# Performance work log

Measured on AMD Instinct MI355X. Metric: run time of the kernel, lower is better.

## Reference

```python
import jax, jax.numpy as jnp
import numpy as np


def setup_inputs() -> dict:
    key = jax.random.key(0)
    ks = jax.random.split(key, 4)
    B, H, W, C = 4, 64, 64, 256
    d = C // 8
    x = jax.random.normal(ks[0], (B, H, W, C), dtype=jnp.float32)
    wq = jax.random.normal(ks[1], (C, d), dtype=jnp.float32) * (1.0 / np.sqrt(C))
    wk = jax.random.normal(ks[2], (C, d), dtype=jnp.float32) * (1.0 / np.sqrt(C))
    wv = jax.random.normal(ks[3], (C, C), dtype=jnp.float32) * (1.0 / np.sqrt(C))
    bq = jnp.zeros((d,), dtype=jnp.float32)
    bk = jnp.zeros((d,), dtype=jnp.float32)
    bv = jnp.zeros((C,), dtype=jnp.float32)
    return {"x": x, "wq": wq, "bq": bq, "wk": wk, "bk": bk, "wv": wv, "bv": bv}


def reference(x, wq, bq, wk, bk, wv, bv):
    # x: [B, H, W, C] (channels-last, as in Keras Conv2D default)
    B, H, W, C = x.shape
    N = H * W
    xf = x.reshape(B, N, C)                      # 1x1 conv == per-pixel matmul
    q = xf @ wq + bq                             # [B, N, C//8]
    k = xf @ wk + bk                             # [B, N, C//8]
    v = xf @ wv + bv                             # [B, N, C]
    # NOTE: original module applies NO 1/sqrt(d) scaling.
    attn = jax.nn.softmax(jnp.einsum('bnd,bmd->bnm', q, k), axis=-1)  # [B, N, N]
    out = jnp.einsum('bnm,bmc->bnc', attn, v)    # [B, N, C]
    return out.reshape(B, H, W, C) + x
```

## Files before the change

### kernel.cpp

```cpp
#include <hip/hip_runtime.h>
#include <stdint.h>

typedef _Float16 f16;
typedef f16 half8 __attribute__((ext_vector_type(8)));
typedef f16 half4 __attribute__((ext_vector_type(4)));
typedef float floatx4 __attribute__((ext_vector_type(4)));

#define MFMA_F16(A, B, Cc) __builtin_amdgcn_mfma_f32_16x16x32_f16((A), (B), (Cc), 0, 0, 0)

static constexpr int NB  = 4;
static constexpr int NN  = 4096;
static constexpr int NC  = 256;
static constexpr int ND  = 32;
static constexpr int PIX = NB * NN;
static constexpr int NS  = 4;
static constexpr int KS  = NN / NS;

__device__ f16 g_WbT[320 * 256];
__device__ f16 g_Qh[(size_t)PIX * ND];
__device__ f16 g_Kh[(size_t)PIX * ND];
__device__ f16 g_VbT[(size_t)NB * NC * NN];
__device__ f16 g_Of[(size_t)NS * PIX * NC];
__device__ float g_m[NS * PIX];
__device__ float g_l[NS * PIX];

__device__ inline void gl2lds16(const f16* g, f16* l) {
  __builtin_amdgcn_global_load_lds(
      (const __attribute__((address_space(1))) void*)g,
      (__attribute__((address_space(3))) void*)l, 16, 0, 0);
}

__global__ __launch_bounds__(256) void prep_weights(const float* __restrict__ wq,
                                                    const float* __restrict__ wk,
                                                    const float* __restrict__ wv) {
  const int tid = blockIdx.x * 256 + threadIdx.x;
  if (tid >= 320 * 256) return;
  const int j = tid >> 8;
  const int k = tid & 255;
  float v;
  if (j < 32)      v = wq[k * 32 + j];
  else if (j < 64) v = wk[k * 32 + (j - 32)];
  else             v = wv[k * 256 + (j - 64)];
  g_WbT[j * 256 + k] = (f16)v;
}

__global__ __launch_bounds__(256) void proj_qkv(const float* __restrict__ x,
                                                const float* __restrict__ bq,
                                                const float* __restrict__ bk,
                                                const float* __restrict__ bv) {
  __shared__ f16 xs[64 * 32];
  __shared__ f16 wsT[320 * 32];
  __shared__ f16 vt[256 * 64];

  const int tid  = threadIdx.x;
  const int lane = tid & 63;
  const int wid  = tid >> 6;
  const int qd   = lane >> 4;
  const int c16  = lane & 15;
  const int p0   = blockIdx.x * 64;
  const floatx4 zero4 = {0.f, 0.f, 0.f, 0.f};

  floatx4 acc[20];
#pragma unroll
  for (int i = 0; i < 20; ++i) acc[i] = zero4;

  for (int kk = 0; kk < 256; kk += 32) {
    {
      const int r = tid >> 2, g = tid & 3;
      const floatx4* s4 = (const floatx4*)(x + (size_t)(p0 + r) * NC + kk + g * 8);
      const floatx4 xa = s4[0], xb = s4[1];
      half8 h;
      h[0] = (f16)xa[0]; h[1] = (f16)xa[1]; h[2] = (f16)xa[2]; h[3] = (f16)xa[3];
      h[4] = (f16)xb[0]; h[5] = (f16)xb[1]; h[6] = (f16)xb[2]; h[7] = (f16)xb[3];
      *(half8*)&xs[r * 32 + g * 8] = h;
    }
#pragma unroll
    for (int i = 0; i < 10; ++i) {
      const int cid = tid + 256 * i;
      const int j = cid >> 3, m = cid & 7;
      *(half4*)&wsT[j * 32 + m * 4] = *(const half4*)&g_WbT[j * 256 + kk + m * 4];
    }
    __syncthreads();
    const half8 a = *(const half8*)&xs[(wid * 16 + c16) * 32 + qd * 8];
#pragma unroll
    for (int nt = 0; nt < 20; ++nt) {
      const half8 bfr = *(const half8*)&wsT[(nt * 16 + c16) * 32 + qd * 8];
      acc[nt] = MFMA_F16(a, bfr, acc[nt]);
    }
    __syncthreads();
  }

#pragma unroll
  for (int nt = 0; nt < 20; ++nt) {
    const int j = nt * 16 + c16;
    const float bias = (j < 32) ? bq[j] : (j < 64) ? bk[j - 32] : bv[j - 64];
#pragma unroll
    for (int r = 0; r < 4; ++r) {
      const int rl = wid * 16 + qd * 4 + r;
      const int p  = p0 + rl;
      const float val = acc[nt][r] + bias;
      if (j < 32) {
        g_Qh[(size_t)p * ND + j] = (f16)(val * 1.44269504f);
      } else if (j < 64) {
        g_Kh[(size_t)p * ND + (j - 32)] = (f16)val;
      } else {
        vt[(j - 64) * 64 + rl] = (f16)val;
      }
    }
  }
  __syncthreads();
  const int b  = p0 >> 12;
  const int n0 = p0 & (NN - 1);
#pragma unroll
  for (int i = 0; i < 16; ++i) {
    const int cid = tid + 256 * i;
    const int c = cid >> 4, m = cid & 15;
    *(half4*)(g_VbT + ((size_t)(b * NC + c)) * NN + n0 + m * 4) =
        *(const half4*)&vt[c * 64 + m * 4];
  }
}

__global__ __launch_bounds__(256, 2) void attn_split(void) {
  __shared__ f16 vsT[256 * 64];
  __shared__ f16 ps[4][2][16 * 64];

  const int tid  = threadIdx.x;
  const int lane = tid & 63;
  const int wid  = tid >> 6;
  const int qd   = lane >> 4;
  const int c16  = lane & 15;
  const int b    = blockIdx.y;
  const int s    = blockIdx.z;
  const int q0   = blockIdx.x * 128 + wid * 32;
  const int sx7  = c16 & 7;
  const floatx4 zero4 = {0.f, 0.f, 0.f, 0.f};

  const int vrow = wid * 64 + (lane >> 3);
  const int vchk = (lane & 7) ^ ((lane >> 3) & 7);
  const f16* vlane = g_VbT + ((size_t)(b * NC + vrow)) * NN + vchk * 8;
  f16* vdst = &vsT[(size_t)wid * 4096 + (size_t)0];

  half8 qf[2];
#pragma unroll
  for (int g = 0; g < 2; ++g)
    qf[g] = *(const half8*)(g_Qh + ((size_t)(b * NN + q0 + g * 16 + c16)) * ND + qd * 8);

  floatx4 acc[2][16];
#pragma unroll
  for (int g = 0; g < 2; ++g)
#pragma unroll
    for (int i = 0; i < 16; ++i) acc[g][i] = zero4;
  float m_i[2] = {-1e30f, -1e30f};
  float l_p[2] = {0.f, 0.f};

  const int kbeg = s * KS, kend = (s + 1) * KS;

#pragma unroll
  for (int i = 0; i < 8; ++i)
    gl2lds16(vlane + kbeg + i * 8 * NN, vdst + i * 512);
  half8 kreg[4];
#pragma unroll
  for (int a = 0; a < 4; ++a)
    kreg[a] = *(const half8*)(g_Kh + ((size_t)(b * NN + kbeg + a * 16 + c16)) * ND + qd * 8);

  for (int k0 = kbeg; k0 < kend; k0 += 64) {
    floatx4 st[2][4];
#pragma unroll
    for (int g = 0; g < 2; ++g)
#pragma unroll
      for (int a = 0; a < 4; ++a) st[g][a] = MFMA_F16(kreg[a], qf[g], zero4);

    float tm[2];
#pragma unroll
    for (int g = 0; g < 2; ++g) {
      float t0 = fmaxf(fmaxf(st[g][0][0], st[g][0][1]), fmaxf(st[g][0][2], st[g][0][3]));
      float t1 = fmaxf(fmaxf(st[g][1][0], st[g][1][1]), fmaxf(st[g][1][2], st[g][1][3]));
      float t2 = fmaxf(fmaxf(st[g][2][0], st[g][2][1]), fmaxf(st[g][2][2], st[g][2][3]));
      float t3 = fmaxf(fmaxf(st[g][3][0], st[g][3][1]), fmaxf(st[g][3][2], st[g][3][3]));
      tm[g] = fmaxf(fmaxf(t0, t1), fmaxf(t2, t3));
    }
    if (__any(tm[0] > m_i[0] || tm[1] > m_i[1])) {
#pragma unroll
      for (int g = 0; g < 2; ++g) {
        float tr = tm[g];
        tr = fmaxf(tr, __shfl_xor(tr, 16));
        tr = fmaxf(tr, __shfl_xor(tr, 32));
        const float m_new = (tr > m_i[g]) ? tr + 5.0f : m_i[g];
        const float alpha = exp2f(m_i[g] - m_new);
        m_i[g] = m_new;
        l_p[g] *= alpha;
        float a4[4];
#pragma unroll
        for (int r = 0; r < 4; ++r) a4[r] = __shfl(alpha, qd * 4 + r);
#pragma unroll
        for (int ct = 0; ct < 16; ++ct)
#pragma unroll
          for (int r = 0; r < 4; ++r) acc[g][ct][r] *= a4[r];
      }
    }

#pragma unroll
    for (int g = 0; g < 2; ++g) {
      float ts = 0.f;
#pragma unroll
      for (int a = 0; a < 4; ++a) {
        half4 h;
#pragma unroll
        for (int r = 0; r < 4; ++r) {
          const float p = exp2f(st[g][a][r] - m_i[g]);
          ts += p;
          h[r] = (f16)p;
        }
        const int pc = ((a * 2 + (qd >> 1)) ^ sx7) * 8 + (qd & 1) * 4;
        *(half4*)&ps[wid][g][c16 * 64 + pc] = h;
      }
      l_p[g] += ts;
    }

    __syncthreads();

    const int k0n = (k0 + 64 < kend) ? (k0 + 64) : kbeg;
    half8 knew[4];
#pragma unroll
    for (int a = 0; a < 4; ++a)
      knew[a] = *(const half8*)(g_Kh + ((size_t)(b * NN + k0n + a * 16 + c16)) * ND + qd * 8);

    half8 pa[2][2];
#pragma unroll
    for (int g = 0; g < 2; ++g)
#pragma unroll
      for (int kh = 0; kh < 2; ++kh)
        pa[g][kh] = *(const half8*)&ps[wid][g][c16 * 64 + ((kh * 4 + qd) ^ sx7) * 8];
#pragma unroll
    for (int ct = 0; ct < 16; ++ct) {
#pragma unroll
      for (int kh = 0; kh < 2; ++kh) {
        const half8 bfr =
            *(const half8*)&vsT[(ct * 16 + c16) * 64 + ((kh * 4 + qd) ^ sx7) * 8];
        acc[0][ct] = MFMA_F16(pa[0][kh], bfr, acc[0][ct]);
        acc[1][ct] = MFMA_F16(pa[1][kh], bfr, acc[1][ct]);
      }
    }
    __syncthreads();

    if (k0 + 64 < kend) {
#pragma unroll
      for (int i = 0; i < 8; ++i)
        gl2lds16(vlane + (k0 + 64) + i * 8 * NN, vdst + i * 512);
    }
#pragma unroll
    for (int a = 0; a < 4; ++a) kreg[a] = knew[a];
  }

#pragma unroll
  for (int g = 0; g < 2; ++g) {
    float l = l_p[g];
    l += __shfl_xor(l, 16);
    l += __shfl_xor(l, 32);
    if (qd == 0) {
      const int row = b * NN + q0 + g * 16 + c16;
      g_m[s * PIX + row] = m_i[g];
      g_l[s * PIX + row] = l;
    }
    float linv[4];
#pragma unroll
    for (int r = 0; r < 4; ++r) linv[r] = 1.0f / __shfl(l, qd * 4 + r);
#pragma unroll
    for (int ct = 0; ct < 16; ++ct)
#pragma unroll
      for (int r = 0; r < 4; ++r) {
        const int qrow = q0 + g * 16 + qd * 4 + r;
        const int c = ct * 16 + c16;
        g_Of[((size_t)(s * PIX + b * NN + qrow)) * NC + c] = (f16)(acc[g][ct][r] * linv[r]);
      }
  }
}

__global__ __launch_bounds__(256) void combine(const float* __restrict__ x,
                                               float* __restrict__ out) {
  const int tid  = threadIdx.x;
  const int lane = tid & 63;
  const int wid  = tid >> 6;
  const int row  = blockIdx.x * 4 + wid;
  const int c    = lane * 4;

  float m[NS], l[NS], M = -1e30f;
#pragma unroll
  for (int s = 0; s < NS; ++s) {
    m[s] = g_m[s * PIX + row];
    l[s] = g_l[s * PIX + row];
    M = fmaxf(M, m[s]);
  }
  float w[NS], den = 0.f;
#pragma unroll
  for (int s = 0; s < NS; ++s) { w[s] = l[s] * exp2f(m[s] - M); den += w[s]; }
  const float inv = 1.0f / den;

  float a0 = 0.f, a1 = 0.f, a2 = 0.f, a3 = 0.f;
#pragma unroll
  for (int s = 0; s < NS; ++s) {
    const half4 h = *(const half4*)&g_Of[((size_t)(s * PIX + row)) * NC + c];
    const float ws = w[s] * inv;
    a0 += ws * (float)h[0];
    a1 += ws * (float)h[1];
    a2 += ws * (float)h[2];
    a3 += ws * (float)h[3];
  }
  const floatx4 xv = *(const floatx4*)&x[(size_t)row * NC + c];
  floatx4 o;
  o[0] = a0 + xv[0]; o[1] = a1 + xv[1]; o[2] = a2 + xv[2]; o[3] = a3 + xv[3];
  *(floatx4*)&out[(size_t)row * NC + c] = o;
}

extern "C" void kernel_launch(void* const* d_in, const int* in_sizes, int n_in,
                              void* d_out, int out_size, void* d_ws, size_t ws_size,
                              hipStream_t stream) {
  (void)in_sizes; (void)n_in; (void)d_ws; (void)ws_size; (void)out_size;
  const float* x  = (const float*)d_in[0];
  const float* wq = (const float*)d_in[1];
  const float* bq = (const float*)d_in[2];
  const float* wk = (const float*)d_in[3];
  const float* bk = (const float*)d_in[4];
  const float* wv = (const float*)d_in[5];
  const float* bv = (const float*)d_in[6];
  float* out = (float*)d_out;

  hipLaunchKernelGGL(prep_weights, dim3(320), dim3(256), 0, stream, wq, wk, wv);
  hipLaunchKernelGGL(proj_qkv, dim3(256), dim3(256), 0, stream, x, bq, bk, bv);
  hipLaunchKernelGGL(attn_split, dim3(NN / 128, NB, NS), dim3(256), 0, stream);
  hipLaunchKernelGGL(combine, dim3(PIX / 4), dim3(256), 0, stream, x, out);
}
```

Measured before the change: 166.2 us.

## Halve per-wave query rows in attention to raise occupancy

```diff
diff --git a/kernel.cpp b/kernel.cpp
--- a/kernel.cpp
+++ b/kernel.cpp
@@ -120,9 +120,9 @@
   }
 }
 
-__global__ __launch_bounds__(256, 2) void attn_split(void) {
+__global__ __launch_bounds__(256, 4) void attn_split(void) {
   __shared__ f16 vsT[256 * 64];
-  __shared__ f16 ps[4][2][16 * 64];
+  __shared__ f16 ps[4][16 * 64];
 
   const int tid  = threadIdx.x;
   const int lane = tid & 63;
@@ -131,27 +131,23 @@
   const int c16  = lane & 15;
   const int b    = blockIdx.y;
   const int s    = blockIdx.z;
-  const int q0   = blockIdx.x * 128 + wid * 32;
+  const int q0   = blockIdx.x * 64 + wid * 16;
   const int sx7  = c16 & 7;
   const floatx4 zero4 = {0.f, 0.f, 0.f, 0.f};
 
   const int vrow = wid * 64 + (lane >> 3);
   const int vchk = (lane & 7) ^ ((lane >> 3) & 7);
   const f16* vlane = g_VbT + ((size_t)(b * NC + vrow)) * NN + vchk * 8;
-  f16* vdst = &vsT[(size_t)wid * 4096 + (size_t)0];
-
-  half8 qf[2];
-#pragma unroll
-  for (int g = 0; g < 2; ++g)
-    qf[g] = *(const half8*)(g_Qh + ((size_t)(b * NN + q0 + g * 16 + c16)) * ND + qd * 8);
-
-  floatx4 acc[2][16];
-#pragma unroll
-  for (int g = 0; g < 2; ++g)
-#pragma unroll
-    for (int i = 0; i < 16; ++i) acc[g][i] = zero4;
-  float m_i[2] = {-1e30f, -1e30f};
-  float l_p[2] = {0.f, 0.f};
+  f16* vdst = &vsT[(size_t)wid * 4096];
+
+  const half8 qf =
+      *(const half8*)(g_Qh + ((size_t)(b * NN + q0 + c16)) * ND + qd * 8);
+
+  floatx4 acc[16];
+#pragma unroll
+  for (int i = 0; i < 16; ++i) acc[i] = zero4;
+  float m_i = -1e30f;
+  float l_p = 0.f;
 
   const int kbeg = s * KS, kend = (s + 1) * KS;
 
@@ -164,81 +160,65 @@
     kreg[a] = *(const half8*)(g_Kh + ((size_t)(b * NN + kbeg + a * 16 + c16)) * ND + qd * 8);
 
   for (int k0 = kbeg; k0 < kend; k0 += 64) {
-    floatx4 st[2][4];
-#pragma unroll
-    for (int g = 0; g < 2; ++g)
-#pragma unroll
-      for (int a = 0; a < 4; ++a) st[g][a] = MFMA_F16(kreg[a], qf[g], zero4);
-
-    float tm[2];
-#pragma unroll
-    for (int g = 0; g < 2; ++g) {
-      float t0 = fmaxf(fmaxf(st[g][0][0], st[g][0][1]), fmaxf(st[g][0][2], st[g][0][3]));
-      float t1 = fmaxf(fmaxf(st[g][1][0], st[g][1][1]), fmaxf(st[g][1][2], st[g][1][3]));
-      float t2 = fmaxf(fmaxf(st[g][2][0], st[g][2][1]), fmaxf(st[g][2][2], st[g][2][3]));
-      float t3 = fmaxf(fmaxf(st[g][3][0], st[g][3][1]), fmaxf(st[g][3][2], st[g][3][3]));
-      tm[g] = fmaxf(fmaxf(t0, t1), fmaxf(t2, t3));
-    }
-    if (__any(tm[0] > m_i[0] || tm[1] > m_i[1])) {
-#pragma unroll
-      for (int g = 0; g < 2; ++g) {
-        float tr = tm[g];
-        tr = fmaxf(tr, __shfl_xor(tr, 16));
-        tr = fmaxf(tr, __shfl_xor(tr, 32));
-        const float m_new = (tr > m_i[g]) ? tr + 5.0f : m_i[g];
-        const float alpha = exp2f(m_i[g] - m_new);
-        m_i[g] = m_new;
-        l_p[g] *= alpha;
-        float a4[4];
-#pragma unroll
-        for (int r = 0; r < 4; ++r) a4[r] = __shfl(alpha, qd * 4 + r);
-#pragma unroll
-        for (int ct = 0; ct < 16; ++ct)
-#pragma unroll
-          for (int r = 0; r < 4; ++r) acc[g][ct][r] *= a4[r];
+    floatx4 st[4];
+#pragma unroll
+    for (int a = 0; a < 4; ++a) st[a] = MFMA_F16(kreg[a], qf, zero4);
+
+    float t0 = fmaxf(fmaxf(st[0][0], st[0][1]), fmaxf(st[0][2], st[0][3]));
+    float t1 = fmaxf(fmaxf(st[1][0], st[1][1]), fmaxf(st[1][2], st[1][3]));
+    float t2 = fmaxf(fmaxf(st[2][0], st[2][1]), fmaxf(st[2][2], st[2][3]));
+    float t3 = fmaxf(fmaxf(st[3][0], st[3][1]), fmaxf(st[3][2], st[3][3]));
+    const float tm = fmaxf(fmaxf(t0, t1), fmaxf(t2, t3));
+    if (__any(tm > m_i)) {
+      float tr = tm;
+      tr = fmaxf(tr, __shfl_xor(tr, 16));
+      tr = fmaxf(tr, __shfl_xor(tr, 32));
+      const float m_new = (tr > m_i) ? tr + 5.0f : m_i;
+      const float alpha = exp2f(m_i - m_new);
+      m_i = m_new;
+      l_p *= alpha;
+      float a4[4];
+#pragma unroll
+      for (int r = 0; r < 4; ++r) a4[r] = __shfl(alpha, qd * 4 + r);
+#pragma unroll
+      for (int ct = 0; ct < 16; ++ct)
+#pragma unroll
+        for (int r = 0; r < 4; ++r) acc[ct][r] *= a4[r];
+    }
+
+    float ts = 0.f;
+#pragma unroll
+    for (int a = 0; a < 4; ++a) {
+      half4 h;
+#pragma unroll
+      for (int r = 0; r < 4; ++r) {
+        const float p = exp2f(st[a][r] - m_i);
+        ts += p;
+        h[r] = (f16)p;
       }
-    }
-
-#pragma unroll
-    for (int g = 0; g < 2; ++g) {
-      float ts = 0.f;
-#pragma unroll
-      for (int a = 0; a < 4; ++a) {
-        half4 h;
-#pragma unroll
-        for (int r = 0; r < 4; ++r) {
-          const float p = exp2f(st[g][a][r] - m_i[g]);
-          ts += p;
-          h[r] = (f16)p;
-        }
-        const int pc = ((a * 2 + (qd >> 1)) ^ sx7) * 8 + (qd & 1) * 4;
-        *(half4*)&ps[wid][g][c16 * 64 + pc] = h;
-      }
-      l_p[g] += ts;
-    }
+      const int pc = ((a * 2 + (qd >> 1)) ^ sx7) * 8 + (qd & 1) * 4;
+      *(half4*)&ps[wid][c16 * 64 + pc] = h;
+    }
+    l_p += ts;
 
     __syncthreads();
 
     const int k0n = (k0 + 64 < kend) ? (k0 + 64) : kbeg;
-    half8 knew[4];
 #pragma unroll
     for (int a = 0; a < 4; ++a)
-      knew[a] = *(const half8*)(g_Kh + ((size_t)(b * NN + k0n + a * 16 + c16)) * ND + qd * 8);
-
-    half8 pa[2][2];
-#pragma unroll
-    for (int g = 0; g < 2; ++g)
-#pragma unroll
-      for (int kh = 0; kh < 2; ++kh)
-        pa[g][kh] = *(const half8*)&ps[wid][g][c16 * 64 + ((kh * 4 + qd) ^ sx7) * 8];
+      kreg[a] = *(const half8*)(g_Kh + ((size_t)(b * NN + k0n + a * 16 + c16)) * ND + qd * 8);
+
+    half8 pa[2];
+#pragma unroll
+    for (int kh = 0; kh < 2; ++kh)
+      pa[kh] = *(const half8*)&ps[wid][c16 * 64 + ((kh * 4 + qd) ^ sx7) * 8];
 #pragma unroll
     for (int ct = 0; ct < 16; ++ct) {
 #pragma unroll
       for (int kh = 0; kh < 2; ++kh) {
         const half8 bfr =
             *(const half8*)&vsT[(ct * 16 + c16) * 64 + ((kh * 4 + qd) ^ sx7) * 8];
-        acc[0][ct] = MFMA_F16(pa[0][kh], bfr, acc[0][ct]);
-        acc[1][ct] = MFMA_F16(pa[1][kh], bfr, acc[1][ct]);
+        acc[ct] = MFMA_F16(pa[kh], bfr, acc[ct]);
       }
     }
     __syncthreads();
@@ -248,18 +228,15 @@
       for (int i = 0; i < 8; ++i)
         gl2lds16(vlane + (k0 + 64) + i * 8 * NN, vdst + i * 512);
     }
-#pragma unroll
-    for (int a = 0; a < 4; ++a) kreg[a] = knew[a];
-  }
-
-#pragma unroll
-  for (int g = 0; g < 2; ++g) {
-    float l = l_p[g];
+  }
+
+  {
+    float l = l_p;
     l += __shfl_xor(l, 16);
     l += __shfl_xor(l, 32);
     if (qd == 0) {
-      const int row = b * NN + q0 + g * 16 + c16;
-      g_m[s * PIX + row] = m_i[g];
+      const int row = b * NN + q0 + c16;
+      g_m[s * PIX + row] = m_i;
       g_l[s * PIX + row] = l;
     }
     float linv[4];
@@ -269,9 +246,9 @@
     for (int ct = 0; ct < 16; ++ct)
 #pragma unroll
       for (int r = 0; r < 4; ++r) {
-        const int qrow = q0 + g * 16 + qd * 4 + r;
+        const int qrow = q0 + qd * 4 + r;
         const int c = ct * 16 + c16;
-        g_Of[((size_t)(s * PIX + b * NN + qrow)) * NC + c] = (f16)(acc[g][ct][r] * linv[r]);
+        g_Of[((size_t)(s * PIX + b * NN + qrow)) * NC + c] = (f16)(acc[ct][r] * linv[r]);
       }
   }
 }
@@ -327,6 +304,6 @@
 
   hipLaunchKernelGGL(prep_weights, dim3(320), dim3(256), 0, stream, wq, wk, wv);
   hipLaunchKernelGGL(proj_qkv, dim3(256), dim3(256), 0, stream, x, bq, bk, bv);
-  hipLaunchKernelGGL(attn_split, dim3(NN / 128, NB, NS), dim3(256), 0, stream);
+  hipLaunchKernelGGL(attn_split, dim3(NN / 64, NB, NS), dim3(256), 0, stream);
   hipLaunchKernelGGL(combine, dim3(PIX / 4), dim3(256), 0, stream, x, out);
 }
```

After: 176.8 us. 6.4% more time.
